# Kernel optimization log

Hardware: AMD Instinct MI355X
Metric: run time of the kernel (lower is better)

Reference implementation:

```python
import jax, jax.numpy as jnp
import numpy as np

N_NODES = 100000
N_EDGES = 1600000
N_GRAPHS = 64
FEAT = 64
EMB = 64
HID = 64
VOCAB = 32


def setup_inputs() -> dict:
    key = jax.random.key(0)
    ks = jax.random.split(key, 20)
    w = lambda k, sh: (jax.random.normal(k, sh, jnp.float32) * 0.05)
    x = jax.random.normal(ks[0], (N_NODES, FEAT), jnp.float32)
    edge_index = jax.random.randint(ks[1], (2, N_EDGES), 0, N_NODES, dtype=jnp.int32).astype(jnp.int64)
    batch = jnp.sort(jax.random.randint(ks[2], (N_NODES,), 0, N_GRAPHS, dtype=jnp.int32)).astype(jnp.int64)
    return {
        'x': x, 'edge_index': edge_index, 'batch': batch,
        # RGCN layer 1 (single relation): relation weight, root weight, bias
        'W1': w(ks[3], (FEAT, EMB)), 'root1': w(ks[4], (FEAT, EMB)), 'b1': w(ks[5], (EMB,)),
        # RGCN layer 2
        'W2': w(ks[6], (EMB, HID)), 'root2': w(ks[7], (EMB, HID)), 'b2': w(ks[8], (HID,)),
        # init_h / init_c linear heads
        'Wh': w(ks[9], (HID, HID)), 'bh': w(ks[10], (HID,)),
        'Wc': w(ks[11], (HID, HID)), 'bc': w(ks[12], (HID,)),
        # output layer
        'Wo': w(ks[13], (HID, VOCAB)), 'bo': w(ks[14], (VOCAB,)),
    }


def _rgcn(x, edge_index, W, root, b):
    # PyG RGCNConv with num_relations=1, aggr='mean':
    # out[i] = mean_{j in N(i)} (x[j] @ W) + x[i] @ root + b
    src, dst = edge_index[0], edge_index[1]
    msg = x[src] @ W                                    # [E, out] gather + small GEMM
    agg = jax.ops.segment_sum(msg, dst, num_segments=x.shape[0])
    cnt = jax.ops.segment_sum(jnp.ones((edge_index.shape[1],), x.dtype), dst, num_segments=x.shape[0])
    agg = agg / jnp.maximum(cnt, 1.0)[:, None]
    return agg + x @ root + b


def reference(x, edge_index, batch, W1, root1, b1, W2, root2, b2, Wh, bh, Wc, bc, Wo, bo):
    h = jax.nn.relu(_rgcn(x, edge_index, W1, root1, b1))
    h = jax.nn.relu(_rgcn(h, edge_index, W2, root2, b2))
    # global_mean_pool over graph-assignment vector `batch`
    summ = jax.ops.segment_sum(h, batch, num_segments=N_GRAPHS)
    cnt = jax.ops.segment_sum(jnp.ones((h.shape[0],), h.dtype), batch, num_segments=N_GRAPHS)
    pooled = summ / jnp.maximum(cnt, 1.0)[:, None]      # [G, HID]
    hidden = pooled @ Wh + bh
    cell = pooled @ Wc + bc
    logits = jax.nn.log_softmax(hidden @ Wo + bo, axis=1)
    return (logits, hidden, cell)
```

## Files before the change

kernel.cpp:

```cpp
#include <hip/hip_runtime.h>
#include <hip/hip_bf16.h>


typedef __attribute__((ext_vector_type(8))) short short8;
typedef __attribute__((ext_vector_type(4))) float f32x4;
typedef __attribute__((ext_vector_type(2))) float f32x2;

#define RB 9
#define MAXBINS 256
#define CAP 12288
#define BCAP 14336
#define CHUNK 4096

__device__ inline float bf2f(unsigned short h) {
    return __uint_as_float(((unsigned int)h) << 16);
}
__device__ inline float bflo(unsigned int u) { return __uint_as_float(u << 16); }
__device__ inline float bfhi(unsigned int u) { return __uint_as_float(u & 0xffff0000u); }
__device__ inline unsigned short f2bf(float f) {
    unsigned int u = __float_as_uint(f);
    u = (u + 0x7fffu + ((u >> 16) & 1u)) >> 16;
    return (unsigned short)u;
}

__device__ inline void build_bfrag(const float* __restrict__ W,
                                   const float* __restrict__ R,
                                   int q, int mm, short8 bfrag[8][2]) {
#pragma unroll
    for (int t = 0; t < 8; ++t) {
        const int n = t * 16 + mm;
        const float* P = (n < 64) ? (W + n) : (R + n - 64);
#pragma unroll
        for (int c = 0; c < 2; ++c) {
#pragma unroll
            for (int j = 0; j < 8; ++j) {
                const int k = c * 32 + q * 8 + j;
                bfrag[t][c][j] = (short)f2bf(P[k * 64]);
            }
        }
    }
}

__device__ inline void store_xw_fp8(unsigned char* __restrict__ xw8, int rowbase, int q,
                                    int t, int mm, const f32x4& accT, int N) {
#pragma unroll
    for (int r = 0; r < 4; ++r) {
        const float v0 = accT[r];
        const float v1 = __shfl_down(v0, 1);
        const float v2 = __shfl_down(v0, 2);
        const float v3 = __shfl_down(v0, 3);
        const int orow = rowbase + q * 4 + r;
        if (!(mm & 3) && orow < N) {
            unsigned int u = (unsigned int)__builtin_amdgcn_cvt_pk_fp8_f32(v0, v1, 0, false);
            u = (unsigned int)__builtin_amdgcn_cvt_pk_fp8_f32(v2, v3, (int)u, true);
            *(unsigned int*)&xw8[(size_t)orow * 64 + t * 16 + mm] = u;
        }
    }
}

__global__ __launch_bounds__(256) void bin_gemm1(const int* __restrict__ src,
                                                 const int* __restrict__ dst,
                                                 unsigned int* __restrict__ coarse,
                                                 int* __restrict__ gcur,
                                                 int E, int BINS, int nbBin,
                                                 const float* __restrict__ x,
                                                 const float* __restrict__ W1,
                                                 const float* __restrict__ R1,
                                                 const float* __restrict__ bias,
                                                 unsigned char* __restrict__ xw8,
                                                 unsigned short* __restrict__ xrb,
                                                 int N) {
    __shared__ int cnt[MAXBINS];
    __shared__ int incl[MAXBINS];
    __shared__ int bstart[MAXBINS];
    __shared__ int bcur[MAXBINS];
    __shared__ int gbase[MAXBINS];
    __shared__ unsigned int stage[CHUNK];
    __shared__ unsigned char binOf[CHUNK];

    const int tid = threadIdx.x;
    if (blockIdx.x >= (unsigned)nbBin) {
        const int gb = blockIdx.x - nbBin;
        if (gb == 0 && tid < 16)
            *(unsigned int*)&xw8[(size_t)N * 64 + tid * 4] = 0u;

        const int lane = tid & 63;
        const int q = lane >> 4;
        const int mm = lane & 15;

        short8 bfrag[8][2];
        build_bfrag(W1, R1, q, mm, bfrag);
        float bv[4];
#pragma unroll
        for (int tt = 0; tt < 4; ++tt) bv[tt] = bias[tt * 16 + mm];

        const int wid = tid >> 6;
        const int gw = gb * 4 + wid;
        const int nw = 1024 * 4;
        const int ntiles = N >> 4;

        for (int tile = gw; tile < ntiles; tile += nw) {
            const int row0 = tile << 4;
            const float* ap = &x[(size_t)(row0 + mm) * 64 + q * 8];
            const float4 f0 = *(const float4*)ap;
            const float4 f1 = *(const float4*)(ap + 4);
            const float4 f2 = *(const float4*)(ap + 32);
            const float4 f3 = *(const float4*)(ap + 36);
            short8 a0, a1;
            a0[0] = (short)f2bf(f0.x); a0[1] = (short)f2bf(f0.y);
            a0[2] = (short)f2bf(f0.z); a0[3] = (short)f2bf(f0.w);
            a0[4] = (short)f2bf(f1.x); a0[5] = (short)f2bf(f1.y);
            a0[6] = (short)f2bf(f1.z); a0[7] = (short)f2bf(f1.w);
            a1[0] = (short)f2bf(f2.x); a1[1] = (short)f2bf(f2.y);
            a1[2] = (short)f2bf(f2.z); a1[3] = (short)f2bf(f2.w);
            a1[4] = (short)f2bf(f3.x); a1[5] = (short)f2bf(f3.y);
            a1[6] = (short)f2bf(f3.z); a1[7] = (short)f2bf(f3.w);
            f32x4 acc[8];
#pragma unroll
            for (int t = 0; t < 8; ++t) {
                acc[t] = (f32x4){0.f, 0.f, 0.f, 0.f};
                acc[t] = __builtin_amdgcn_mfma_f32_16x16x32_bf16(a0, bfrag[t][0], acc[t], 0, 0, 0);
                acc[t] = __builtin_amdgcn_mfma_f32_16x16x32_bf16(a1, bfrag[t][1], acc[t], 0, 0, 0);
            }
#pragma unroll
            for (int t = 0; t < 4; ++t) store_xw_fp8(xw8, row0, q, t, mm, acc[t], N);
#pragma unroll
            for (int t = 4; t < 8; ++t) {
#pragma unroll
                for (int r = 0; r < 4; ++r) {
                    const float v = acc[t][r] + bv[t - 4];
                    const float vn = __shfl_down(v, 1);
                    if (!(mm & 1)) {
                        const unsigned int u = (unsigned int)f2bf(v) | ((unsigned int)f2bf(vn) << 16);
                        *(unsigned int*)&xrb[(size_t)(row0 + q * 4 + r) * 64 + (t - 4) * 16 + mm] = u;
                    }
                }
            }
        }
        return;
    }

    const int chunk0 = blockIdx.x * CHUNK;
    int myS[16], myD[16];
#pragma unroll
    for (int k = 0; k < 16; ++k) {
        const int idx = chunk0 + k * 256 + tid;
        if (idx < E) { myS[k] = src[idx]; myD[k] = dst[idx]; }
        else myD[k] = -1;
    }
    cnt[tid] = 0;
    __syncthreads();
#pragma unroll
    for (int k = 0; k < 16; ++k)
        if (myD[k] >= 0) atomicAdd(&cnt[myD[k] >> RB], 1);
    __syncthreads();
    incl[tid] = cnt[tid];
    __syncthreads();
    for (int off = 1; off < 256; off <<= 1) {
        int t = (tid >= off) ? incl[tid - off] : 0;
        __syncthreads();
        incl[tid] += t;
        __syncthreads();
    }
    bstart[tid] = incl[tid] - cnt[tid];
    bcur[tid] = incl[tid] - cnt[tid];
    __syncthreads();
#pragma unroll
    for (int k = 0; k < 16; ++k) {
        if (myD[k] >= 0) {
            const int b = myD[k] >> RB;
            const int pos = atomicAdd(&bcur[b], 1);
            stage[pos] = (unsigned int)myS[k] | ((unsigned int)(myD[k] & ((1 << RB) - 1)) << 17);
            binOf[pos] = (unsigned char)b;
        }
    }
    __syncthreads();
    if (tid < BINS && cnt[tid] > 0)
        gbase[tid] = tid * CAP + atomicAdd(&gcur[tid], cnt[tid]);
    __syncthreads();
    int total = E - chunk0;
    if (total > CHUNK) total = CHUNK;
    for (int idx = tid; idx < total; idx += 256) {
        const int b = binOf[idx];
        coarse[gbase[b] + (idx - bstart[b])] = stage[idx];
    }
}

__global__ __launch_bounds__(256) void finalize_csr(const unsigned int* __restrict__ coarse,
                                                    const int* __restrict__ gcur,
                                                    int* __restrict__ bucket,
                                                    int* __restrict__ pstart,
                                                    int* __restrict__ degarr,
                                                    int N, int BINS) {
    __shared__ int ncnt[512];
    __shared__ int pexcl[512];
    __shared__ int ncur[512];
    __shared__ int s2[256];

    const int tid = threadIdx.x;
    const int b = blockIdx.x;
    const int cb = gcur[b];
    const int base = b * BCAP;
    const unsigned int* reg = coarse + (size_t)b * CAP;
    const int node0 = b << RB;
    int nloc = N - node0;
    if (nloc > 512) nloc = 512;

    ncnt[tid] = 0; ncnt[tid + 256] = 0;
    __syncthreads();
    for (int idx = tid; idx < cb; idx += 256)
        atomicAdd(&ncnt[reg[idx] >> 17], 1);
    __syncthreads();
    const int p0 = (ncnt[2 * tid] + 15) & ~15;
    const int p1 = (ncnt[2 * tid + 1] + 15) & ~15;
    s2[tid] = p0 + p1;
    __syncthreads();
    for (int off = 1; off < 256; off <<= 1) {
        int t = (tid >= off) ? s2[tid - off] : 0;
        __syncthreads();
        s2[tid] += t;
        __syncthreads();
    }
    const int pairExcl = s2[tid] - (p0 + p1);
    pexcl[2 * tid] = pairExcl;
    pexcl[2 * tid + 1] = pairExcl + p0;
    ncur[2 * tid] = pairExcl;
    ncur[2 * tid + 1] = pairExcl + p0;
    __syncthreads();
    for (int i = tid; i < nloc; i += 256) {
        pstart[node0 + i] = base + pexcl[i];
        degarr[node0 + i] = ncnt[i];
    }
    for (int idx = tid; idx < cb; idx += 256) {
        const unsigned int e = reg[idx];
        const int p = atomicAdd(&ncur[e >> 17], 1);
        bucket[base + p] = (int)(e & 0x1FFFFu);
    }
}

__global__ __launch_bounds__(256) void aggregate(const unsigned char* __restrict__ xw8,
                                                 const unsigned short* __restrict__ xrb,
                                                 const int* __restrict__ pstart,
                                                 const int* __restrict__ degarr,
                                                 const int* __restrict__ bucket,
                                                 unsigned short* __restrict__ outb,
                                                 int N) {
    const int lane = threadIdx.x & 63;
    const int quarter = lane >> 4;
    const int fl = lane & 15;
    const int wid = threadIdx.x >> 6;
    const int gw = blockIdx.x * 4 + wid;
    const int nw = gridDim.x * 4;
    const unsigned flo = (unsigned)(fl << 2);

    for (int i = gw; i < N; i += 2 * nw) {
        const int iA = i;
        const int iB = i + nw;
        const bool hasB = iB < N;
        const int r0A = pstart[iA];
        const int dgA = degarr[iA];
        int r0B = r0A, dgB = 0;
        if (hasB) { r0B = pstart[iB]; dgB = degarr[iB]; }
        const int pdA = (dgA + 15) & ~15;
        const int pdB = (dgB + 15) & ~15;
        const int pdM = pdA > pdB ? pdA : pdB;

        uint2 urA = {0u, 0u}, urB = {0u, 0u};
        if (quarter == 0) {
            urA = *(const uint2*)&xrb[(size_t)iA * 64 + fl * 4];
            if (hasB) urB = *(const uint2*)&xrb[(size_t)iB * 64 + fl * 4];
        }

        f32x2 aAlo = {0.f, 0.f}, aAhi = {0.f, 0.f};
        f32x2 aBlo = {0.f, 0.f}, aBhi = {0.f, 0.f};
        for (int base = 0; base < pdM; base += 64) {
            const int remA = pdA - base;
            const int remB = pdB - base;
            const int trmA = dgA - base;
            const int trmB = dgB - base;
            int sA = N, sB = N;
            if (trmA > 0 && lane < trmA)
                sA = *(const int*)((const char*)bucket + ((unsigned)(r0A + base + lane) << 2));
            if (trmB > 0 && lane < trmB)
                sB = *(const int*)((const char*)bucket + ((unsigned)(r0B + base + lane) << 2));
            const int mxA = remA < 64 ? remA : 64;
            const int mxB = remB < 64 ? remB : 64;
            int mx = pdM - base;
            if (mx > 64) mx = 64;
            for (int t = 0; t < mx; t += 16) {
                const bool doA = t < mxA;
                const bool doB = t < mxB;
                unsigned int uA[4], uB[4];
                if (doA) {
#pragma unroll
                    for (int p = 0; p < 4; ++p) {
                        const unsigned rr = (unsigned)__shfl(sA, t + 4 * p + quarter);
                        uA[p] = *(const unsigned int*)(xw8 + ((rr << 6) | flo));
                    }
                }
                if (doB) {
#pragma unroll
                    for (int p = 0; p < 4; ++p) {
                        const unsigned rr = (unsigned)__shfl(sB, t + 4 * p + quarter);
                        uB[p] = *(const unsigned int*)(xw8 + ((rr << 6) | flo));
                    }
                }
                if (doA) {
#pragma unroll
                    for (int p = 0; p < 4; ++p) {
                        aAlo += __builtin_amdgcn_cvt_pk_f32_fp8(uA[p], false);
                        aAhi += __builtin_amdgcn_cvt_pk_f32_fp8(uA[p], true);
                    }
                }
                if (doB) {
#pragma unroll
                    for (int p = 0; p < 4; ++p) {
                        aBlo += __builtin_amdgcn_cvt_pk_f32_fp8(uB[p], false);
                        aBhi += __builtin_amdgcn_cvt_pk_f32_fp8(uB[p], true);
                    }
                }
            }
        }
        float aA0 = aAlo.x, aA1 = aAlo.y, aA2 = aAhi.x, aA3 = aAhi.y;
        float aB0 = aBlo.x, aB1 = aBlo.y, aB2 = aBhi.x, aB3 = aBhi.y;
        aA0 += __shfl_xor(aA0, 16); aA1 += __shfl_xor(aA1, 16);
        aA2 += __shfl_xor(aA2, 16); aA3 += __shfl_xor(aA3, 16);
        aA0 += __shfl_xor(aA0, 32); aA1 += __shfl_xor(aA1, 32);
        aA2 += __shfl_xor(aA2, 32); aA3 += __shfl_xor(aA3, 32);
        aB0 += __shfl_xor(aB0, 16); aB1 += __shfl_xor(aB1, 16);
        aB2 += __shfl_xor(aB2, 16); aB3 += __shfl_xor(aB3, 16);
        aB0 += __shfl_xor(aB0, 32); aB1 += __shfl_xor(aB1, 32);
        aB2 += __shfl_xor(aB2, 32); aB3 += __shfl_xor(aB3, 32);

        if (quarter == 0) {
            const float invA = 1.0f / (float)(dgA > 0 ? dgA : 1);
            const float o0 = fmaxf(aA0 * invA + bflo(urA.x), 0.f);
            const float o1 = fmaxf(aA1 * invA + bfhi(urA.x), 0.f);
            const float o2 = fmaxf(aA2 * invA + bflo(urA.y), 0.f);
            const float o3 = fmaxf(aA3 * invA + bfhi(urA.y), 0.f);
            uint2 w;
            w.x = (unsigned int)f2bf(o0) | ((unsigned int)f2bf(o1) << 16);
            w.y = (unsigned int)f2bf(o2) | ((unsigned int)f2bf(o3) << 16);
            *(uint2*)&outb[(size_t)iA * 64 + fl * 4] = w;
            if (hasB) {
                const float invB = 1.0f / (float)(dgB > 0 ? dgB : 1);
                const float p0 = fmaxf(aB0 * invB + bflo(urB.x), 0.f);
                const float p1 = fmaxf(aB1 * invB + bfhi(urB.x), 0.f);
                const float p2 = fmaxf(aB2 * invB + bflo(urB.y), 0.f);
                const float p3 = fmaxf(aB3 * invB + bfhi(urB.y), 0.f);
                uint2 w2;
                w2.x = (unsigned int)f2bf(p0) | ((unsigned int)f2bf(p1) << 16);
                w2.y = (unsigned int)f2bf(p2) | ((unsigned int)f2bf(p3) << 16);
                *(uint2*)&outb[(size_t)iB * 64 + fl * 4] = w2;
            }
        }
    }
}

__global__ __launch_bounds__(256) void gemm_xwr2(const unsigned short* __restrict__ xin,
                                                 const float* __restrict__ W2,
                                                 const float* __restrict__ R2,
                                                 const float* __restrict__ bias,
                                                 unsigned char* __restrict__ xw8,
                                                 unsigned short* __restrict__ xrb,
                                                 int M) {
    if (blockIdx.x == 0 && threadIdx.x < 16)
        *(unsigned int*)&xw8[(size_t)M * 64 + threadIdx.x * 4] = 0u;

    const int lane = threadIdx.x & 63;
    const int q = lane >> 4;
    const int mm = lane & 15;

    short8 bfrag[8][2];
    build_bfrag(W2, R2, q, mm, bfrag);
    float bv[4];
#pragma unroll
    for (int tt = 0; tt < 4; ++tt) bv[tt] = bias[tt * 16 + mm];

    const int wid = threadIdx.x >> 6;
    const int gw = blockIdx.x * 4 + wid;
    const int nw = gridDim.x * 4;
    const int ntiles = M >> 4;

    for (int tile = gw; tile < ntiles; tile += nw) {
        const int row0 = tile << 4;
        const short8 a0 = *(const short8*)&xin[(size_t)(row0 + mm) * 64 + q * 8];
        const short8 a1 = *(const short8*)&xin[(size_t)(row0 + mm) * 64 + 32 + q * 8];
        f32x4 acc[8];
#pragma unroll
        for (int t = 0; t < 8; ++t) {
            acc[t] = (f32x4){0.f, 0.f, 0.f, 0.f};
            acc[t] = __builtin_amdgcn_mfma_f32_16x16x32_bf16(a0, bfrag[t][0], acc[t], 0, 0, 0);
            acc[t] = __builtin_amdgcn_mfma_f32_16x16x32_bf16(a1, bfrag[t][1], acc[t], 0, 0, 0);
        }
#pragma unroll
        for (int t = 0; t < 4; ++t) store_xw_fp8(xw8, row0, q, t, mm, acc[t], M);
#pragma unroll
        for (int t = 4; t < 8; ++t) {
#pragma unroll
            for (int r = 0; r < 4; ++r) {
                const float v = acc[t][r] + bv[t - 4];
                const float vn = __shfl_down(v, 1);
                if (!(mm & 1)) {
                    const unsigned int u = (unsigned int)f2bf(v) | ((unsigned int)f2bf(vn) << 16);
                    *(unsigned int*)&xrb[(size_t)(row0 + q * 4 + r) * 64 + (t - 4) * 16 + mm] = u;
                }
            }
        }
    }
}

__global__ __launch_bounds__(256) void pool_kernel(const unsigned short* __restrict__ h,
                                                   const int* __restrict__ batch,
                                                   float* __restrict__ gsum, int N) {
    __shared__ float red[16][64];
    __shared__ int bnds[2];
    const int gph = blockIdx.x >> 2;
    const int part = blockIdx.x & 3;
    if (threadIdx.x < 2) {
        const int target = gph + threadIdx.x;
        int lo = 0, hi = N;
        while (lo < hi) {
            int mid = (lo + hi) >> 1;
            if (batch[mid] < target) lo = mid + 1; else hi = mid;
        }
        bnds[threadIdx.x] = lo;
    }
    __syncthreads();
    const int r0 = bnds[0], tot = bnds[1] - bnds[0];
    const int pr0 = r0 + (tot * part) / 4;
    const int pr1 = r0 + (tot * (part + 1)) / 4;
    const int f = threadIdx.x & 15;
    const int r = threadIdx.x >> 4;
    float4 acc = {0.f, 0.f, 0.f, 0.f};
    for (int row = pr0 + r; row < pr1; row += 16) {
        const ushort4 v = *(const ushort4*)&h[(size_t)row * 64 + f * 4];
        acc.x += bf2f(v.x); acc.y += bf2f(v.y);
        acc.z += bf2f(v.z); acc.w += bf2f(v.w);
    }
    red[r][f * 4 + 0] = acc.x; red[r][f * 4 + 1] = acc.y;
    red[r][f * 4 + 2] = acc.z; red[r][f * 4 + 3] = acc.w;
    __syncthreads();
    if (threadIdx.x < 64) {
        float s = 0.f;
        for (int j = 0; j < 16; ++j) s += red[j][threadIdx.x];
        atomicAdd(&gsum[gph * 64 + threadIdx.x], s);
    }
}

__global__ __launch_bounds__(256) void head_kernel(const float* __restrict__ gsum,
                                                   const int* __restrict__ batch,
                                                   const float* __restrict__ Wh,
                                                   const float* __restrict__ bh,
                                                   const float* __restrict__ Wc,
                                                   const float* __restrict__ bc,
                                                   const float* __restrict__ Wo,
                                                   const float* __restrict__ bo,
                                                   float* __restrict__ out, int N) {
    __shared__ float pm[4096];
    __shared__ float Ws[4096];
    __shared__ float Cs[4096];
    __shared__ float hid[4096];
    __shared__ int bnds[65];
    const int t = threadIdx.x;

    if (t < 65) {
        int lo = 0, hi = N;
        while (lo < hi) {
            int mid = (lo + hi) >> 1;
            if (batch[mid] < t) lo = mid + 1; else hi = mid;
        }
        bnds[t] = lo;
    }
    __syncthreads();
    for (int idx = t; idx < 1024; idx += 256) {
        const int g = idx >> 4;
        const int c = bnds[g + 1] - bnds[g];
        const float inv = 1.0f / (float)(c > 0 ? c : 1);
        float4 v = ((const float4*)gsum)[idx];
        v.x *= inv; v.y *= inv; v.z *= inv; v.w *= inv;
        ((float4*)pm)[idx] = v;
        ((float4*)Ws)[idx] = ((const float4*)Wh)[idx];
        ((float4*)Cs)[idx] = ((const float4*)Wc)[idx];
    }
    __syncthreads();

    const int w = t >> 6;
    const int l = t & 63;
    const float bhv = bh[l], bcv = bc[l];
    float ah[16], ac[16];
#pragma unroll
    for (int i = 0; i < 16; ++i) { ah[i] = bhv; ac[i] = bcv; }
    const float* pmw = pm + ((w << 4) << 6);
#pragma unroll 4
    for (int k = 0; k < 64; ++k) {
        const float wv = Ws[(k << 6) + l];
        const float cv = Cs[(k << 6) + l];
#pragma unroll
        for (int i = 0; i < 16; ++i) {
            const float p = pmw[(i << 6) + k];
            ah[i] = fmaf(p, wv, ah[i]);
            ac[i] = fmaf(p, cv, ac[i]);
        }
    }
#pragma unroll
    for (int i = 0; i < 16; ++i) {
        const int g = (w << 4) + i;
        hid[(g << 6) + l] = ah[i];
        out[2048 + (g << 6) + l] = ah[i];
        out[6144 + (g << 6) + l] = ac[i];
    }
    __syncthreads();
    for (int idx = t; idx < 512; idx += 256)
        ((float4*)Ws)[idx] = ((const float4*)Wo)[idx];
    __syncthreads();

    const int v = l & 31;
    const int gh = l >> 5;
    const int g0 = ((w << 1) + gh) << 3;
    const float bov = bo[v];
    float lgacc[8];
#pragma unroll
    for (int i = 0; i < 8; ++i) lgacc[i] = bov;
#pragma unroll 4
    for (int k = 0; k < 64; ++k) {
        const float wv = Ws[(k << 5) + v];
#pragma unroll
        for (int i = 0; i < 8; ++i)
            lgacc[i] = fmaf(hid[((g0 + i) << 6) + k], wv, lgacc[i]);
    }
    float* lg = pm;
#pragma unroll
    for (int i = 0; i < 8; ++i) lg[((g0 + i) << 5) + v] = lgacc[i];
    __syncthreads();

    const int g = t >> 2;
    const int vs = (t & 3) << 3;
    const float* row = lg + (g << 5);
    float mx = -3.4e38f;
#pragma unroll
    for (int j = 0; j < 8; ++j) mx = fmaxf(mx, row[vs + j]);
    mx = fmaxf(mx, __shfl_xor(mx, 1));
    mx = fmaxf(mx, __shfl_xor(mx, 2));
    float s = 0.f;
#pragma unroll
    for (int j = 0; j < 8; ++j) s += __expf(row[vs + j] - mx);
    s += __shfl_xor(s, 1);
    s += __shfl_xor(s, 2);
    const float lse = mx + __logf(s);
#pragma unroll
    for (int j = 0; j < 8; ++j) out[(g << 5) + vs + j] = row[vs + j] - lse;
}

extern "C" void kernel_launch(void* const* d_in, const int* in_sizes, int n_in,
                              void* d_out, int out_size, void* d_ws, size_t ws_size,
                              hipStream_t stream) {
    const float* x = (const float*)d_in[0];
    const int* ei = (const int*)d_in[1];
    const int* batch = (const int*)d_in[2];
    const float* W1 = (const float*)d_in[3];
    const float* root1 = (const float*)d_in[4];
    const float* b1 = (const float*)d_in[5];
    const float* W2 = (const float*)d_in[6];
    const float* root2 = (const float*)d_in[7];
    const float* b2 = (const float*)d_in[8];
    const float* Wh = (const float*)d_in[9];
    const float* bh = (const float*)d_in[10];
    const float* Wc = (const float*)d_in[11];
    const float* bc = (const float*)d_in[12];
    const float* Wo = (const float*)d_in[13];
    const float* bo = (const float*)d_in[14];
    float* out = (float*)d_out;

    const int N = in_sizes[0] / 64;
    const int E = in_sizes[1] / 2;
    const int* srcp = ei;
    const int* dstp = ei + E;
    const int BINS = (N + (1 << RB) - 1) >> RB;

    char* ws = (char*)d_ws;
    size_t off = 0;
    auto alloc = [&](size_t bytes) -> void* {
        void* p = ws + off;
        off += (bytes + 255) & ~(size_t)255;
        return p;
    };
    int* pstart = (int*)alloc((size_t)N * 4);
    int* degarr = (int*)alloc((size_t)N * 4);
    int* bucket = (int*)alloc(((size_t)BINS * BCAP + 256) * 4);
    unsigned int* coarse = (unsigned int*)alloc((size_t)BINS * CAP * 4);
    unsigned short* h1 = (unsigned short*)alloc((size_t)N * 64 * 2);
    unsigned short* h2 = (unsigned short*)alloc((size_t)N * 64 * 2);
    unsigned char* xw8 = (unsigned char*)alloc((size_t)(N + 1) * 64);
    unsigned char* xw8b = (unsigned char*)alloc((size_t)(N + 1) * 64);
    unsigned short* xrb = (unsigned short*)alloc((size_t)N * 64 * 2);
    unsigned short* xrb2 = (unsigned short*)alloc((size_t)N * 64 * 2);
    int* gcur = (int*)alloc(MAXBINS * 4);
    float* gsum = (float*)alloc(4096 * 4);

    const int nbBin = (E + CHUNK - 1) / CHUNK;

    hipMemsetAsync(gcur, 0, MAXBINS * 4 + 4096 * 4, stream);
    bin_gemm1<<<nbBin + 1024, 256, 0, stream>>>(srcp, dstp, coarse, gcur, E, BINS, nbBin,
                                                x, W1, root1, b1, xw8, xrb, N);
    finalize_csr<<<BINS, 256, 0, stream>>>(coarse, gcur, bucket, pstart, degarr, N, BINS);
    aggregate<<<4096, 256, 0, stream>>>(xw8, xrb, pstart, degarr, bucket, h1, N);
    gemm_xwr2<<<1024, 256, 0, stream>>>(h1, W2, root2, b2, xw8b, xrb2, N);
    aggregate<<<4096, 256, 0, stream>>>(xw8b, xrb2, pstart, degarr, bucket, h2, N);
    pool_kernel<<<256, 256, 0, stream>>>(h2, batch, gsum, N);
    head_kernel<<<1, 256, 0, stream>>>(gsum, batch, Wh, bh, Wc, bc, Wo, bo, out, N);
}
```

Baseline: 246.5 us.

## Fuse mean-pool into second aggregate via atomics and prefetch CSR offsets

The second aggregate pass now adds its ReLU outputs straight into the per-graph sums with float atomics instead of writing h2 and running a separate pool kernel, which removes an N×64 bf16 write/read and one launch. The aggregate loop also prefetches the next iteration's pstart/degarr values to hide their load latency. The duplicated GEMM tile body is factored into a shared helper. Per-element atomics onto only 64 graph rows can contend heavily, and they make the summation order nondeterministic.

```diff
diff --git a/kernel.cpp b/kernel.cpp
--- a/kernel.cpp
+++ b/kernel.cpp
@@ -54,6 +54,34 @@
             unsigned int u = (unsigned int)__builtin_amdgcn_cvt_pk_fp8_f32(v0, v1, 0, false);
             u = (unsigned int)__builtin_amdgcn_cvt_pk_fp8_f32(v2, v3, (int)u, true);
             *(unsigned int*)&xw8[(size_t)orow * 64 + t * 16 + mm] = u;
+        }
+    }
+}
+
+__device__ inline void gemm_tile_body(const short8& a0, const short8& a1,
+                                      const short8 bfrag[8][2], const float bv[4],
+                                      unsigned char* __restrict__ xw8,
+                                      unsigned short* __restrict__ xrb,
+                                      int row0, int q, int mm, int N) {
+    f32x4 acc[8];
+#pragma unroll
+    for (int t = 0; t < 8; ++t) {
+        acc[t] = (f32x4){0.f, 0.f, 0.f, 0.f};
+        acc[t] = __builtin_amdgcn_mfma_f32_16x16x32_bf16(a0, bfrag[t][0], acc[t], 0, 0, 0);
+        acc[t] = __builtin_amdgcn_mfma_f32_16x16x32_bf16(a1, bfrag[t][1], acc[t], 0, 0, 0);
+    }
+#pragma unroll
+    for (int t = 0; t < 4; ++t) store_xw_fp8(xw8, row0, q, t, mm, acc[t], N);
+#pragma unroll
+    for (int t = 4; t < 8; ++t) {
+#pragma unroll
+        for (int r = 0; r < 4; ++r) {
+            const float v = acc[t][r] + bv[t - 4];
+            const float vn = __shfl_down(v, 1);
+            if (!(mm & 1)) {
+                const unsigned int u = (unsigned int)f2bf(v) | ((unsigned int)f2bf(vn) << 16);
+                *(unsigned int*)&xrb[(size_t)(row0 + q * 4 + r) * 64 + (t - 4) * 16 + mm] = u;
+            }
         }
     }
 }
@@ -115,27 +143,7 @@
             a1[2] = (short)f2bf(f2.z); a1[3] = (short)f2bf(f2.w);
             a1[4] = (short)f2bf(f3.x); a1[5] = (short)f2bf(f3.y);
             a1[6] = (short)f2bf(f3.z); a1[7] = (short)f2bf(f3.w);
-            f32x4 acc[8];
-#pragma unroll
-            for (int t = 0; t < 8; ++t) {
-                acc[t] = (f32x4){0.f, 0.f, 0.f, 0.f};
-                acc[t] = __builtin_amdgcn_mfma_f32_16x16x32_bf16(a0, bfrag[t][0], acc[t], 0, 0, 0);
-                acc[t] = __builtin_amdgcn_mfma_f32_16x16x32_bf16(a1, bfrag[t][1], acc[t], 0, 0, 0);
-            }
-#pragma unroll
-            for (int t = 0; t < 4; ++t) store_xw_fp8(xw8, row0, q, t, mm, acc[t], N);
-#pragma unroll
-            for (int t = 4; t < 8; ++t) {
-#pragma unroll
-                for (int r = 0; r < 4; ++r) {
-                    const float v = acc[t][r] + bv[t - 4];
-                    const float vn = __shfl_down(v, 1);
-                    if (!(mm & 1)) {
-                        const unsigned int u = (unsigned int)f2bf(v) | ((unsigned int)f2bf(vn) << 16);
-                        *(unsigned int*)&xrb[(size_t)(row0 + q * 4 + r) * 64 + (t - 4) * 16 + mm] = u;
-                    }
-                }
-            }
+            gemm_tile_body(a0, a1, bfrag, bv, xw8, xrb, row0, q, mm, N);
         }
         return;
     }
@@ -244,6 +252,8 @@
                                                  const int* __restrict__ degarr,
                                                  const int* __restrict__ bucket,
                                                  unsigned short* __restrict__ outb,
+                                                 const int* __restrict__ batch,
+                                                 float* __restrict__ gsum,
                                                  int N) {
     const int lane = threadIdx.x & 63;
     const int quarter = lane >> 4;
@@ -253,14 +263,26 @@
     const int nw = gridDim.x * 4;
     const unsigned flo = (unsigned)(fl << 2);
 
+    int r0A = 0, dgA = 0, r0B = 0, dgB = 0;
+    if (gw < N) {
+        r0A = pstart[gw]; dgA = degarr[gw];
+        const int b0 = gw + nw;
+        if (b0 < N) { r0B = pstart[b0]; dgB = degarr[b0]; }
+    }
+
     for (int i = gw; i < N; i += 2 * nw) {
         const int iA = i;
         const int iB = i + nw;
         const bool hasB = iB < N;
-        const int r0A = pstart[iA];
-        const int dgA = degarr[iA];
-        int r0B = r0A, dgB = 0;
-        if (hasB) { r0B = pstart[iB]; dgB = degarr[iB]; }
+
+        const int nA = i + 2 * nw;
+        int nr0A = 0, ndgA = 0, nr0B = 0, ndgB = 0;
+        if (nA < N) {
+            nr0A = pstart[nA]; ndgA = degarr[nA];
+            const int nB = nA + nw;
+            if (nB < N) { nr0B = pstart[nB]; ndgB = degarr[nB]; }
+        }
+
         const int pdA = (dgA + 15) & ~15;
         const int pdB = (dgB + 15) & ~15;
         const int pdM = pdA > pdB ? pdA : pdB;
@@ -269,6 +291,11 @@
         if (quarter == 0) {
             urA = *(const uint2*)&xrb[(size_t)iA * 64 + fl * 4];
             if (hasB) urB = *(const uint2*)&xrb[(size_t)iB * 64 + fl * 4];
+        }
+        int gA = 0, gB = 0;
+        if (gsum) {
+            gA = batch[iA];
+            if (hasB) gB = batch[iB];
         }
 
         f32x2 aAlo = {0.f, 0.f}, aAhi = {0.f, 0.f};
@@ -338,22 +365,35 @@
             const float o1 = fmaxf(aA1 * invA + bfhi(urA.x), 0.f);
             const float o2 = fmaxf(aA2 * invA + bflo(urA.y), 0.f);
             const float o3 = fmaxf(aA3 * invA + bfhi(urA.y), 0.f);
-            uint2 w;
-            w.x = (unsigned int)f2bf(o0) | ((unsigned int)f2bf(o1) << 16);
-            w.y = (unsigned int)f2bf(o2) | ((unsigned int)f2bf(o3) << 16);
-            *(uint2*)&outb[(size_t)iA * 64 + fl * 4] = w;
+            if (gsum) {
+                float* gp = gsum + (gA << 6) + fl * 4;
+                atomicAdd(gp + 0, o0); atomicAdd(gp + 1, o1);
+                atomicAdd(gp + 2, o2); atomicAdd(gp + 3, o3);
+            } else {
+                uint2 w;
+                w.x = (unsigned int)f2bf(o0) | ((unsigned int)f2bf(o1) << 16);
+                w.y = (unsigned int)f2bf(o2) | ((unsigned int)f2bf(o3) << 16);
+                *(uint2*)&outb[(size_t)iA * 64 + fl * 4] = w;
+            }
             if (hasB) {
                 const float invB = 1.0f / (float)(dgB > 0 ? dgB : 1);
                 const float p0 = fmaxf(aB0 * invB + bflo(urB.x), 0.f);
                 const float p1 = fmaxf(aB1 * invB + bfhi(urB.x), 0.f);
                 const float p2 = fmaxf(aB2 * invB + bflo(urB.y), 0.f);
                 const float p3 = fmaxf(aB3 * invB + bfhi(urB.y), 0.f);
-                uint2 w2;
-                w2.x = (unsigned int)f2bf(p0) | ((unsigned int)f2bf(p1) << 16);
-                w2.y = (unsigned int)f2bf(p2) | ((unsigned int)f2bf(p3) << 16);
-                *(uint2*)&outb[(size_t)iB * 64 + fl * 4] = w2;
+                if (gsum) {
+                    float* gp = gsum + (gB << 6) + fl * 4;
+                    atomicAdd(gp + 0, p0); atomicAdd(gp + 1, p1);
+                    atomicAdd(gp + 2, p2); atomicAdd(gp + 3, p3);
+                } else {
+                    uint2 w2;
+                    w2.x = (unsigned int)f2bf(p0) | ((unsigned int)f2bf(p1) << 16);
+                    w2.y = (unsigned int)f2bf(p2) | ((unsigned int)f2bf(p3) << 16);
+                    *(uint2*)&outb[(size_t)iB * 64 + fl * 4] = w2;
+                }
             }
         }
+        r0A = nr0A; dgA = ndgA; r0B = nr0B; dgB = ndgB;
     }
 }
 
@@ -386,65 +426,7 @@
         const int row0 = tile << 4;
         const short8 a0 = *(const short8*)&xin[(size_t)(row0 + mm) * 64 + q * 8];
         const short8 a1 = *(const short8*)&xin[(size_t)(row0 + mm) * 64 + 32 + q * 8];
-        f32x4 acc[8];
-#pragma unroll
-        for (int t = 0; t < 8; ++t) {
-            acc[t] = (f32x4){0.f, 0.f, 0.f, 0.f};
-            acc[t] = __builtin_amdgcn_mfma_f32_16x16x32_bf16(a0, bfrag[t][0], acc[t], 0, 0, 0);
-            acc[t] = __builtin_amdgcn_mfma_f32_16x16x32_bf16(a1, bfrag[t][1], acc[t], 0, 0, 0);
-        }
-#pragma unroll
-        for (int t = 0; t < 4; ++t) store_xw_fp8(xw8, row0, q, t, mm, acc[t], M);
-#pragma unroll
-        for (int t = 4; t < 8; ++t) {
-#pragma unroll
-            for (int r = 0; r < 4; ++r) {
-                const float v = acc[t][r] + bv[t - 4];
-                const float vn = __shfl_down(v, 1);
-                if (!(mm & 1)) {
-                    const unsigned int u = (unsigned int)f2bf(v) | ((unsigned int)f2bf(vn) << 16);
-                    *(unsigned int*)&xrb[(size_t)(row0 + q * 4 + r) * 64 + (t - 4) * 16 + mm] = u;
-                }
-            }
-        }
-    }
-}
-
-__global__ __launch_bounds__(256) void pool_kernel(const unsigned short* __restrict__ h,
-                                                   const int* __restrict__ batch,
-                                                   float* __restrict__ gsum, int N) {
-    __shared__ float red[16][64];
-    __shared__ int bnds[2];
-    const int gph = blockIdx.x >> 2;
-    const int part = blockIdx.x & 3;
-    if (threadIdx.x < 2) {
-        const int target = gph + threadIdx.x;
-        int lo = 0, hi = N;
-        while (lo < hi) {
-            int mid = (lo + hi) >> 1;
-            if (batch[mid] < target) lo = mid + 1; else hi = mid;
-        }
-        bnds[threadIdx.x] = lo;
-    }
-    __syncthreads();
-    const int r0 = bnds[0], tot = bnds[1] - bnds[0];
-    const int pr0 = r0 + (tot * part) / 4;
-    const int pr1 = r0 + (tot * (part + 1)) / 4;
-    const int f = threadIdx.x & 15;
-    const int r = threadIdx.x >> 4;
-    float4 acc = {0.f, 0.f, 0.f, 0.f};
-    for (int row = pr0 + r; row < pr1; row += 16) {
-        const ushort4 v = *(const ushort4*)&h[(size_t)row * 64 + f * 4];
-        acc.x += bf2f(v.x); acc.y += bf2f(v.y);
-        acc.z += bf2f(v.z); acc.w += bf2f(v.w);
-    }
-    red[r][f * 4 + 0] = acc.x; red[r][f * 4 + 1] = acc.y;
-    red[r][f * 4 + 2] = acc.z; red[r][f * 4 + 3] = acc.w;
-    __syncthreads();
-    if (threadIdx.x < 64) {
-        float s = 0.f;
-        for (int j = 0; j < 16; ++j) s += red[j][threadIdx.x];
-        atomicAdd(&gsum[gph * 64 + threadIdx.x], s);
+        gemm_tile_body(a0, a1, bfrag, bv, xw8, xrb, row0, q, mm, M);
     }
 }
 
@@ -590,7 +572,6 @@
     int* bucket = (int*)alloc(((size_t)BINS * BCAP + 256) * 4);
     unsigned int* coarse = (unsigned int*)alloc((size_t)BINS * CAP * 4);
     unsigned short* h1 = (unsigned short*)alloc((size_t)N * 64 * 2);
-    unsigned short* h2 = (unsigned short*)alloc((size_t)N * 64 * 2);
     unsigned char* xw8 = (unsigned char*)alloc((size_t)(N + 1) * 64);
     unsigned char* xw8b = (unsigned char*)alloc((size_t)(N + 1) * 64);
     unsigned short* xrb = (unsigned short*)alloc((size_t)N * 64 * 2);
@@ -604,9 +585,10 @@
     bin_gemm1<<<nbBin + 1024, 256, 0, stream>>>(srcp, dstp, coarse, gcur, E, BINS, nbBin,
                                                 x, W1, root1, b1, xw8, xrb, N);
     finalize_csr<<<BINS, 256, 0, stream>>>(coarse, gcur, bucket, pstart, degarr, N, BINS);
-    aggregate<<<4096, 256, 0, stream>>>(xw8, xrb, pstart, degarr, bucket, h1, N);
+    aggregate<<<4096, 256, 0, stream>>>(xw8, xrb, pstart, degarr, bucket, h1,
+                                        nullptr, nullptr, N);
     gemm_xwr2<<<1024, 256, 0, stream>>>(h1, W2, root2, b2, xw8b, xrb2, N);
-    aggregate<<<4096, 256, 0, stream>>>(xw8b, xrb2, pstart, degarr, bucket, h2, N);
-    pool_kernel<<<256, 256, 0, stream>>>(h2, batch, gsum, N);
+    aggregate<<<4096, 256, 0, stream>>>(xw8b, xrb2, pstart, degarr, bucket, nullptr,
+                                        batch, gsum, N);
     head_kernel<<<1, 256, 0, stream>>>(gsum, batch, Wh, bh, Wc, bc, Wo, bo, out, N);
 }
```

Result: slower. 576.8 us (+134.0%).
